# Kernel optimization log

Measured on AMD Instinct MI355X. Metric: run time of the kernel, lower is better.

## Reference

```python
import jax, jax.numpy as jnp
import numpy as np

# ---- module config (mirrors arch_args / init_kwargs) ----
W_BITS_PER_SLICE = 4      # slice_init=True -> weights quantized with STE to w_bits_per_slice
A_BITS = 8                # activation quantization bits
A_BITS_PER_STREAM = 8
VMAX = 1.0
GON_HW, GOFF_HW = 1.0, 1e-3   # weight_to_diff_conductance is called with Gon=1, Goff=1/1000 (hardcoded)
ADC_PREC = 8
ADC_STEP = 1e-3           # adc_static_step
NUM_SUBARRAYS = 9
SUB_SIZE = 256            # subarray_size; 256*3*3 / 256 = 9 even chunks
K, STRIDE, PAD = 3, 1, 1


def ste_quantize(x, bits):
    # Symmetric uniform quantizer with straight-through estimator (STE_Quantize).
    n = float(2 ** bits - 1)
    s = jnp.max(jnp.abs(x)) + 1e-12
    q = jnp.round(x / s * n) / n * s
    return x + jax.lax.stop_gradient(q - x)


def adc_quantize(I):
    # Nbit_ADC: static-step uniform ADC, signed (adc_pos_only=False), deterministic
    # rounding (adc_stoch_round=False), STE backward, no custom loss.
    half = 2 ** (ADC_PREC - 1)
    q = jnp.clip(jnp.round(I / ADC_STEP), -half, half - 1) * ADC_STEP
    return I + jax.lax.stop_gradient(q - I)


def setup_inputs():
    key = jax.random.key(0)
    k1, k2 = jax.random.split(key)
    x = jax.random.normal(k1, (32, 256, 32, 32), jnp.float32)
    fan_in = 256 * K * K
    w = jax.random.normal(k2, (256, 256, K, K), jnp.float32) * np.sqrt(2.0 / fan_in)  # kaiming_normal
    return {"inputs": x, "weight": w}


def reference(inputs, weight):
    B = inputs.shape[0]
    O = weight.shape[0]

    # forward(): quantize activations (a_bits) and weights (w_bits_per_slice, slice_init path)
    qa = ste_quantize(inputs, A_BITS)
    qw = ste_quantize(weight, W_BITS_PER_SLICE)

    # F.unfold -> [B, C*k*k, L], channel-major patch ordering (matches torch)
    patches = jax.lax.conv_general_dilated_patches(
        qa, (K, K), (STRIDE, STRIDE), ((PAD, PAD), (PAD, PAD)))
    Hp, Wp = patches.shape[2], patches.shape[3]
    L = Hp * Wp
    V = patches.reshape(B, NUM_SUBARRAYS, SUB_SIZE, L) * (VMAX / A_BITS_PER_STREAM)

    # Differential conductances: G_pos - G_neg. The dummy columns (both filled with
    # Goff) cancel exactly in I_pos - I_neg, so the net current per subarray is a
    # single contraction against qw * (Gon - Goff) / Nstates_slice.
    nstates = float(2 ** W_BITS_PER_SLICE - 1)
    Gd = qw.reshape(O, NUM_SUBARRAYS, SUB_SIZE) * ((GON_HW - GOFF_HW) / nstates)

    # per-subarray crossbar currents: [B, n_sub, O, L]
    I = jnp.einsum('bgfl,ogf->bgol', V, Gd)

    # shared ADC applied to each subarray output, then accumulate over subarrays
    accum = adc_quantize(I).sum(axis=1)  # [B, O, L]
    a_loss = jnp.float32(0.0)            # adc_custom_loss=False

    # F.fold with (1,1) kernel onto sqrt(L) x sqrt(L) grid == reshape
    result = accum.reshape(B, O, Hp, Wp)
    return (result, a_loss)
```

## Files before the change

kernel.cpp:

```cpp
#include <hip/hip_runtime.h>
#include <stdint.h>

typedef unsigned short u16;
typedef __attribute__((ext_vector_type(8))) short short8;
typedef __attribute__((ext_vector_type(4))) float floatx4;

#define NB 32
#define NC 256
#define NH 32
#define NW 32
#define NO 256
#define NPIX (NH*NW)
#define KPIX 9
#define NG 9
#define RUN 32
#define GK (NG*RUN)
#define KTOT (NG*GK)
#define PADH 34
#define PADSP (PADH*PADH)
#define QA_BSTRIDE (PADSP*NC)

#define AS1 __attribute__((address_space(1)))
#define AS3 __attribute__((address_space(3)))

__global__ void fused_pre(const float4* __restrict__ x4, int nx4,
                          const float4* __restrict__ w4, int nw4,
                          unsigned* __restrict__ outx, unsigned* __restrict__ outw,
                          u16* __restrict__ qa) {
  int bid = blockIdx.x;
  if (bid >= 1088) {
    int zb = bid - 1088;
    int b = zb / 9;
    int rem = (zb % 9) * 256 + threadIdx.x;
    if (rem >= 2112) return;
    int pb = rem >> 4, c16 = rem & 15;
    int y, x;
    if (pb < 68) { y = (pb >= 34) ? 33 : 0; x = pb % 34; }
    else { int q = pb - 68; y = 1 + (q >> 1); x = (q & 1) ? 33 : 0; }
    uint4 z; z.x = z.y = z.z = z.w = 0u;
    *(uint4*)(qa + ((size_t)(b * PADH + y) * PADH + x) * NC + c16 * 16) = z;
    return;
  }
  const float4* p; int n4; unsigned* out; int nb, b0;
  if (bid < 1024) { p = x4; n4 = nx4; out = outx; nb = 1024; b0 = bid; }
  else            { p = w4; n4 = nw4; out = outw; nb = 64;   b0 = bid - 1024; }
  float m = 0.f;
  for (int i = b0 * blockDim.x + threadIdx.x; i < n4; i += nb * blockDim.x) {
    float4 v = p[i];
    m = fmaxf(m, fmaxf(fmaxf(fabsf(v.x), fabsf(v.y)), fmaxf(fabsf(v.z), fabsf(v.w))));
  }
#pragma unroll
  for (int off = 32; off > 0; off >>= 1)
    m = fmaxf(m, __shfl_down(m, off, 64));
  __shared__ float sm[4];
  int lane = threadIdx.x & 63, wv = threadIdx.x >> 6;
  if (lane == 0) sm[wv] = m;
  __syncthreads();
  if (threadIdx.x == 0) {
    float mm = fmaxf(fmaxf(sm[0], sm[1]), fmaxf(sm[2], sm[3]));
    atomicMax(out, __float_as_uint(mm));
  }
}

__global__ void fused_quant(const float* __restrict__ x, const float* __restrict__ w,
                            const unsigned* __restrict__ scal,
                            u16* __restrict__ qa, u16* __restrict__ wq,
                            float* __restrict__ lossp) {
  int bid = blockIdx.x;
  if (bid < 8192) {
    __shared__ u16 t[32][33];
    double s = (double)__uint_as_float(scal[0]) + 1e-12;
    double inv = 255.0 / s;
    int tx = threadIdx.x & 31, ty = threadIdx.x >> 5;
    int ct = bid & 7, y = (bid >> 3) & 31, b = bid >> 8;
#pragma unroll
    for (int j = 0; j < 4; j++) {
      int cl = ty + j * 8;
      float v = x[(((size_t)b * NC + ct * 32 + cl) * NH + y) * NW + tx];
      double q = rint((double)v * inv);
      float qf = (float)q;
      t[cl][tx] = (u16)(__float_as_uint(qf) >> 16);
    }
    __syncthreads();
#pragma unroll
    for (int j = 0; j < 4; j++) {
      int xq = ty + j * 8;
      qa[((size_t)(b * PADH + y + 1) * PADH + (xq + 1)) * NC + ct * 32 + tx] = t[tx][xq];
    }
    return;
  }
  double s = (double)__uint_as_float(scal[1]) + 1e-12;
  double inv = 15.0 / s;
  int idx = (bid - 8192) * blockDim.x + threadIdx.x;
  if (idx == 0) *lossp = 0.0f;
  if (idx >= NO * KTOT) return;
  int o = idx / KTOT, kk = idx % KTOT;
  int g = kk / GK, rem = kk % GK;
  int r = rem / RUN, j = rem % RUN;
  int clo = (256 * g - r + 8) / 9;
  int chi = (256 * (g + 1) - r + 8) / 9; if (chi > NC) chi = NC;
  int cst = clo & ~3;
  int c = cst + j;
  float val = 0.f;
  if (c >= clo && c < chi) {
    float wv = w[((size_t)o * NC + c) * KPIX + r];
    val = (float)rint((double)wv * inv);
  }
  wq[idx] = (u16)(__float_as_uint(val) >> 16);
}

__global__ __launch_bounds__(128, 2) void gemm_adc(const u16* __restrict__ qa,
                                                   const u16* __restrict__ wq,
                                                   const unsigned* __restrict__ sc,
                                                   float* __restrict__ out) {
  __shared__ u16 lA[3 * 128 * RUN];
  __shared__ u16 lB[3 * 64 * RUN];
  const int tid = threadIdx.x;
  const int mblk = blockIdx.x, nblk = blockIdx.y;
  const int b = mblk >> 3;
  const int p0 = (mblk & 7) * 128;
  const int n0 = nblk * 64;
  const int lane = tid & 63, w = tid >> 6;
  const int fm = lane & 15, fq = lane >> 4;
  const int swz = (fq + ((fm >> 1) & 3)) & 3;

  double sa = (double)__uint_as_float(sc[0]) + 1e-12;
  double sw = (double)__uint_as_float(sc[1]) + 1e-12;
  double Sstep = sa * sw * 0.999 / 459.0;

  const int r0 = tid >> 2;
  const int jsrc = ((tid & 3) - ((tid >> 3) & 3)) & 3;
  const u16* Abase = qa + (size_t)b * QA_BSTRIDE
                     + (((p0 >> 5) + 1) * PADH + (r0 + 1)) * NC + jsrc * 8;
  const u16* Bbase = wq + (size_t)(n0 + r0) * KTOT + jsrc * 8;
  u16* Adst = &lA[tid * 8];
  u16* Bdst = &lB[tid * 8];

  floatx4 acc[4][4];
  float tot[4][4][4];
#pragma unroll
  for (int mi = 0; mi < 4; mi++)
#pragma unroll
    for (int ni = 0; ni < 4; ni++)
#pragma unroll
      for (int rr = 0; rr < 4; rr++) { acc[mi][ni][rr] = 0.f; tot[mi][ni][rr] = 0.f; }

#pragma unroll 1
  for (int g = 0; g < NG; g++) {
#pragma unroll 1
    for (int rc = 0; rc < 3; rc++) {
      int offA[3], kb[3];
#pragma unroll
      for (int ri = 0; ri < 3; ri++) {
        int r = rc * 3 + ri;
        int cst = ((256 * g - r + 8) / 9) & ~3;
        offA[ri] = ((rc - 1) * PADH + (ri - 1)) * NC + cst;
        kb[ri] = g * GK + r * RUN;
      }
#pragma unroll
      for (int ri = 0; ri < 3; ri++)
#pragma unroll
        for (int ii = 0; ii < 4; ii++)
          __builtin_amdgcn_global_load_lds(
              (const AS1 void*)(Abase + offA[ri] + ii * (PADH * NC)),
              (AS3 void*)(Adst + ri * 4096 + ii * 1024), 16, 0, 0);
#pragma unroll
      for (int ii = 0; ii < 6; ii++)
        __builtin_amdgcn_global_load_lds(
            (const AS1 void*)(Bbase + (ii & 1) * 32 * KTOT + kb[ii >> 1]),
            (AS3 void*)(Bdst + ii * 1024), 16, 0, 0);
      __syncthreads();
#pragma unroll
      for (int ri = 0; ri < 3; ri++) {
        short8 afr[4], bfr[4];
#pragma unroll
        for (int mi = 0; mi < 4; mi++)
          afr[mi] = *(const short8*)&lA[ri * 4096 + (w * 64 + mi * 16 + fm) * RUN + swz * 8];
#pragma unroll
        for (int ni = 0; ni < 4; ni++)
          bfr[ni] = *(const short8*)&lB[ri * 2048 + (ni * 16 + fm) * RUN + swz * 8];
#pragma unroll
        for (int mi = 0; mi < 4; mi++)
#pragma unroll
          for (int ni = 0; ni < 4; ni++)
            acc[mi][ni] = __builtin_amdgcn_mfma_f32_16x16x32_bf16(afr[mi], bfr[ni], acc[mi][ni], 0, 0, 0);
      }
      __syncthreads();
    }
#pragma unroll
    for (int mi = 0; mi < 4; mi++)
#pragma unroll
      for (int ni = 0; ni < 4; ni++)
#pragma unroll
        for (int rr = 0; rr < 4; rr++) {
          double d = (double)acc[mi][ni][rr] * Sstep;
          float tf = (float)rint(d);
          tf = fminf(fmaxf(tf, -128.f), 127.f);
          tot[mi][ni][rr] += tf;
          acc[mi][ni][rr] = 0.f;
        }
  }
#pragma unroll
  for (int mi = 0; mi < 4; mi++)
#pragma unroll
    for (int ni = 0; ni < 4; ni++) {
      int o = n0 + ni * 16 + fm;
      int p = p0 + w * 64 + mi * 16 + fq * 4;
      float4 o4;
      o4.x = tot[mi][ni][0] * 1e-3f;
      o4.y = tot[mi][ni][1] * 1e-3f;
      o4.z = tot[mi][ni][2] * 1e-3f;
      o4.w = tot[mi][ni][3] * 1e-3f;
      *(float4*)(out + ((size_t)(b * NO + o)) * NPIX + p) = o4;
    }
}

extern "C" void kernel_launch(void* const* d_in, const int* in_sizes, int n_in,
                              void* d_out, int out_size, void* d_ws, size_t ws_size,
                              hipStream_t stream) {
  const float* x = (const float*)d_in[0];
  const float* w = (const float*)d_in[1];
  float* out = (float*)d_out;

  unsigned* scal = (unsigned*)d_ws;
  u16* qa = (u16*)((char*)d_ws + 256);
  u16* wq = (u16*)((char*)d_ws + 256 + 18939904 + 8192);

  hipMemsetAsync(d_ws, 0, 256, stream);
  fused_pre<<<1376, 256, 0, stream>>>((const float4*)x, (NB * NC * NH * NW) / 4,
                                      (const float4*)w, (NO * NC * KPIX) / 4,
                                      scal, scal + 1, qa);
  fused_quant<<<8192 + 2592, 256, 0, stream>>>(x, w, scal, qa, wq, out + (out_size - 1));
  gemm_adc<<<dim3(256, 4), 128, 0, stream>>>(qa, wq, scal, out);
}
```

Before: 177.0 us.

## Double-buffer GEMM K-loop, replace atomic max with per-block partials, swap grid order

The GEMM main loop now walks 41 chunks of two kernel-pixel slices each and keeps two LDS buffers. The next chunk's async global-to-LDS loads are issued before the current chunk is computed, with explicit vmcnt waits, so memory traffic overlaps the MFMA work. The row stride of the weight matrix is padded to 2624 so the extra 82nd slice reads zeros. The global atomicMax and the memset are replaced by per-block partial maxima, which every block of the quant and GEMM kernels reduces again on its own. The grid is transposed so the N blocks sharing one A tile launch next to each other, which should improve L2 reuse. The costs are twice the LDS use, a redundant reduction in every block, and inline-asm waitcnt logic that is fragile.

Result: slower. 226.6 us (+28.1%).

```diff
diff --git a/kernel.cpp b/kernel.cpp
--- a/kernel.cpp
+++ b/kernel.cpp
@@ -16,6 +16,7 @@
 #define RUN 32
 #define GK (NG*RUN)
 #define KTOT (NG*GK)
+#define KSTORE 2624
 #define PADH 34
 #define PADSP (PADH*PADH)
 #define QA_BSTRIDE (PADSP*NC)
@@ -25,8 +26,7 @@
 
 __global__ void fused_pre(const float4* __restrict__ x4, int nx4,
                           const float4* __restrict__ w4, int nw4,
-                          unsigned* __restrict__ outx, unsigned* __restrict__ outw,
-                          u16* __restrict__ qa) {
+                          float* __restrict__ pmax, u16* __restrict__ qa) {
   int bid = blockIdx.x;
   if (bid >= 1088) {
     int zb = bid - 1088;
@@ -41,9 +41,9 @@
     *(uint4*)(qa + ((size_t)(b * PADH + y) * PADH + x) * NC + c16 * 16) = z;
     return;
   }
-  const float4* p; int n4; unsigned* out; int nb, b0;
-  if (bid < 1024) { p = x4; n4 = nx4; out = outx; nb = 1024; b0 = bid; }
-  else            { p = w4; n4 = nw4; out = outw; nb = 64;   b0 = bid - 1024; }
+  const float4* p; int n4; int nb, b0;
+  if (bid < 1024) { p = x4; n4 = nx4; nb = 1024; b0 = bid; }
+  else            { p = w4; n4 = nw4; nb = 64;   b0 = bid - 1024; }
   float m = 0.f;
   for (int i = b0 * blockDim.x + threadIdx.x; i < n4; i += nb * blockDim.x) {
     float4 v = p[i];
@@ -56,20 +56,46 @@
   int lane = threadIdx.x & 63, wv = threadIdx.x >> 6;
   if (lane == 0) sm[wv] = m;
   __syncthreads();
-  if (threadIdx.x == 0) {
-    float mm = fmaxf(fmaxf(sm[0], sm[1]), fmaxf(sm[2], sm[3]));
-    atomicMax(out, __float_as_uint(mm));
-  }
+  if (threadIdx.x == 0)
+    pmax[bid] = fmaxf(fmaxf(sm[0], sm[1]), fmaxf(sm[2], sm[3]));
+}
+
+__device__ inline void reduce_pmax(const float* pmax, int tid, int nthreads,
+                                   float* sred, float& mx_out, float& mw_out) {
+  const float4* pf4 = (const float4*)pmax;
+  float mx = 0.f, mw = 0.f;
+  for (int t = tid; t < 256; t += nthreads) {
+    float4 v = pf4[t];
+    mx = fmaxf(mx, fmaxf(fmaxf(v.x, v.y), fmaxf(v.z, v.w)));
+  }
+  if (tid < 16) {
+    float4 v = pf4[256 + tid];
+    mw = fmaxf(fmaxf(v.x, v.y), fmaxf(v.z, v.w));
+  }
+#pragma unroll
+  for (int off = 32; off > 0; off >>= 1) {
+    mx = fmaxf(mx, __shfl_down(mx, off, 64));
+    mw = fmaxf(mw, __shfl_down(mw, off, 64));
+  }
+  int lane = tid & 63, wv = tid >> 6, nw = nthreads >> 6;
+  if (lane == 0) { sred[wv] = mx; sred[8 + wv] = mw; }
+  __syncthreads();
+  mx = sred[0]; mw = sred[8];
+  for (int i = 1; i < nw; i++) { mx = fmaxf(mx, sred[i]); mw = fmaxf(mw, sred[8 + i]); }
+  mx_out = mx; mw_out = mw;
 }
 
 __global__ void fused_quant(const float* __restrict__ x, const float* __restrict__ w,
-                            const unsigned* __restrict__ scal,
+                            const float* __restrict__ pmax,
                             u16* __restrict__ qa, u16* __restrict__ wq,
                             float* __restrict__ lossp) {
+  __shared__ float sred[16];
+  float mx, mw;
+  reduce_pmax(pmax, threadIdx.x, 256, sred, mx, mw);
   int bid = blockIdx.x;
   if (bid < 8192) {
     __shared__ u16 t[32][33];
-    double s = (double)__uint_as_float(scal[0]) + 1e-12;
+    double s = (double)mx + 1e-12;
     double inv = 255.0 / s;
     int tx = threadIdx.x & 31, ty = threadIdx.x >> 5;
     int ct = bid & 7, y = (bid >> 3) & 31, b = bid >> 8;
@@ -89,52 +115,78 @@
     }
     return;
   }
-  double s = (double)__uint_as_float(scal[1]) + 1e-12;
+  double s = (double)mw + 1e-12;
   double inv = 15.0 / s;
   int idx = (bid - 8192) * blockDim.x + threadIdx.x;
   if (idx == 0) *lossp = 0.0f;
-  if (idx >= NO * KTOT) return;
-  int o = idx / KTOT, kk = idx % KTOT;
-  int g = kk / GK, rem = kk % GK;
-  int r = rem / RUN, j = rem % RUN;
-  int clo = (256 * g - r + 8) / 9;
-  int chi = (256 * (g + 1) - r + 8) / 9; if (chi > NC) chi = NC;
-  int cst = clo & ~3;
-  int c = cst + j;
+  if (idx >= NO * KSTORE) return;
+  int o = idx / KSTORE, kk = idx % KSTORE;
   float val = 0.f;
-  if (c >= clo && c < chi) {
-    float wv = w[((size_t)o * NC + c) * KPIX + r];
-    val = (float)rint((double)wv * inv);
+  if (kk < KTOT) {
+    int g = kk / GK, rem = kk % GK;
+    int r = rem / RUN, j = rem % RUN;
+    int clo = (256 * g - r + 8) / 9;
+    int chi = (256 * (g + 1) - r + 8) / 9; if (chi > NC) chi = NC;
+    int cst = clo & ~3;
+    int c = cst + j;
+    if (c >= clo && c < chi) {
+      float wv = w[((size_t)o * NC + c) * KPIX + r];
+      val = (float)rint((double)wv * inv);
+    }
   }
   wq[idx] = (u16)(__float_as_uint(val) >> 16);
 }
 
 __global__ __launch_bounds__(128, 2) void gemm_adc(const u16* __restrict__ qa,
                                                    const u16* __restrict__ wq,
-                                                   const unsigned* __restrict__ sc,
+                                                   const float* __restrict__ pmax,
                                                    float* __restrict__ out) {
-  __shared__ u16 lA[3 * 128 * RUN];
-  __shared__ u16 lB[3 * 64 * RUN];
+  __shared__ u16 lA[2 * 2 * 128 * RUN];
+  __shared__ u16 lB[2 * 2 * 64 * RUN];
+  __shared__ float sred[16];
   const int tid = threadIdx.x;
-  const int mblk = blockIdx.x, nblk = blockIdx.y;
+  float mx, mw;
+  reduce_pmax(pmax, tid, 128, sred, mx, mw);
+
+  const int nblk = blockIdx.x, mblk = blockIdx.y;
   const int b = mblk >> 3;
   const int p0 = (mblk & 7) * 128;
   const int n0 = nblk * 64;
-  const int lane = tid & 63, w = tid >> 6;
+  const int lane = tid & 63, wv = tid >> 6;
   const int fm = lane & 15, fq = lane >> 4;
   const int swz = (fq + ((fm >> 1) & 3)) & 3;
 
-  double sa = (double)__uint_as_float(sc[0]) + 1e-12;
-  double sw = (double)__uint_as_float(sc[1]) + 1e-12;
+  double sa = (double)mx + 1e-12;
+  double sw = (double)mw + 1e-12;
   double Sstep = sa * sw * 0.999 / 459.0;
 
   const int r0 = tid >> 2;
   const int jsrc = ((tid & 3) - ((tid >> 3) & 3)) & 3;
   const u16* Abase = qa + (size_t)b * QA_BSTRIDE
                      + (((p0 >> 5) + 1) * PADH + (r0 + 1)) * NC + jsrc * 8;
-  const u16* Bbase = wq + (size_t)(n0 + r0) * KTOT + jsrc * 8;
-  u16* Adst = &lA[tid * 8];
-  u16* Bdst = &lB[tid * 8];
+  const u16* Bbase = wq + (size_t)(n0 + r0) * KSTORE + jsrc * 8;
+
+  auto issue = [&](int c, int buf) {
+#pragma unroll
+    for (int rl = 0; rl < 2; rl++) {
+      int r = 2 * c + rl;
+      int ra = (r >= 81) ? 80 : r;
+      int g = ra / 9, rr = ra % 9;
+      int cst = ((256 * g - rr + 8) / 9) & ~3;
+      int offA = ((rr / 3 - 1) * PADH + (rr % 3 - 1)) * NC + cst;
+      int offB = r * RUN;
+      u16* Ad = &lA[buf * 8192 + rl * 4096 + tid * 8];
+      u16* Bd = &lB[buf * 4096 + rl * 2048 + tid * 8];
+#pragma unroll
+      for (int ii = 0; ii < 4; ii++)
+        __builtin_amdgcn_global_load_lds((const AS1 void*)(Abase + offA + ii * (PADH * NC)),
+                                         (AS3 void*)(Ad + ii * 1024), 16, 0, 0);
+#pragma unroll
+      for (int ii = 0; ii < 2; ii++)
+        __builtin_amdgcn_global_load_lds((const AS1 void*)(Bbase + offB + ii * 32 * KSTORE),
+                                         (AS3 void*)(Bd + ii * 1024), 16, 0, 0);
+    }
+  };
 
   floatx4 acc[4][4];
   float tot[4][4][4];
@@ -145,67 +197,60 @@
 #pragma unroll
       for (int rr = 0; rr < 4; rr++) { acc[mi][ni][rr] = 0.f; tot[mi][ni][rr] = 0.f; }
 
+  issue(0, 0);
 #pragma unroll 1
-  for (int g = 0; g < NG; g++) {
-#pragma unroll 1
-    for (int rc = 0; rc < 3; rc++) {
-      int offA[3], kb[3];
-#pragma unroll
-      for (int ri = 0; ri < 3; ri++) {
-        int r = rc * 3 + ri;
-        int cst = ((256 * g - r + 8) / 9) & ~3;
-        offA[ri] = ((rc - 1) * PADH + (ri - 1)) * NC + cst;
-        kb[ri] = g * GK + r * RUN;
+  for (int c = 0; c < 41; c++) {
+    if (c < 40) {
+      issue(c + 1, (c + 1) & 1);
+      asm volatile("s_waitcnt vmcnt(12)" ::: "memory");
+    } else {
+      asm volatile("s_waitcnt vmcnt(0)" ::: "memory");
+    }
+    __builtin_amdgcn_s_barrier();
+    asm volatile("" ::: "memory");
+    const int buf = c & 1;
+#pragma unroll
+    for (int rl = 0; rl < 2; rl++) {
+      const u16* pA = &lA[buf * 8192 + rl * 4096];
+      const u16* pB = &lB[buf * 4096 + rl * 2048];
+      short8 afr[4], bfr[4];
+#pragma unroll
+      for (int mi = 0; mi < 4; mi++)
+        afr[mi] = *(const short8*)&pA[(wv * 64 + mi * 16 + fm) * RUN + swz * 8];
+#pragma unroll
+      for (int ni = 0; ni < 4; ni++)
+        bfr[ni] = *(const short8*)&pB[(ni * 16 + fm) * RUN + swz * 8];
+#pragma unroll
+      for (int mi = 0; mi < 4; mi++)
+#pragma unroll
+        for (int ni = 0; ni < 4; ni++)
+          acc[mi][ni] = __builtin_amdgcn_mfma_f32_16x16x32_bf16(afr[mi], bfr[ni], acc[mi][ni], 0, 0, 0);
+      int r = 2 * c + rl;
+      if (r % 9 == 8) {
+#pragma unroll
+        for (int mi = 0; mi < 4; mi++)
+#pragma unroll
+          for (int ni = 0; ni < 4; ni++)
+#pragma unroll
+            for (int rr = 0; rr < 4; rr++) {
+              double d = (double)acc[mi][ni][rr] * Sstep;
+              float tf = (float)rint(d);
+              tf = fminf(fmaxf(tf, -128.f), 127.f);
+              tot[mi][ni][rr] += tf;
+              acc[mi][ni][rr] = 0.f;
+            }
       }
-#pragma unroll
-      for (int ri = 0; ri < 3; ri++)
-#pragma unroll
-        for (int ii = 0; ii < 4; ii++)
-          __builtin_amdgcn_global_load_lds(
-              (const AS1 void*)(Abase + offA[ri] + ii * (PADH * NC)),
-              (AS3 void*)(Adst + ri * 4096 + ii * 1024), 16, 0, 0);
-#pragma unroll
-      for (int ii = 0; ii < 6; ii++)
-        __builtin_amdgcn_global_load_lds(
-            (const AS1 void*)(Bbase + (ii & 1) * 32 * KTOT + kb[ii >> 1]),
-            (AS3 void*)(Bdst + ii * 1024), 16, 0, 0);
-      __syncthreads();
-#pragma unroll
-      for (int ri = 0; ri < 3; ri++) {
-        short8 afr[4], bfr[4];
-#pragma unroll
-        for (int mi = 0; mi < 4; mi++)
-          afr[mi] = *(const short8*)&lA[ri * 4096 + (w * 64 + mi * 16 + fm) * RUN + swz * 8];
-#pragma unroll
-        for (int ni = 0; ni < 4; ni++)
-          bfr[ni] = *(const short8*)&lB[ri * 2048 + (ni * 16 + fm) * RUN + swz * 8];
-#pragma unroll
-        for (int mi = 0; mi < 4; mi++)
-#pragma unroll
-          for (int ni = 0; ni < 4; ni++)
-            acc[mi][ni] = __builtin_amdgcn_mfma_f32_16x16x32_bf16(afr[mi], bfr[ni], acc[mi][ni], 0, 0, 0);
-      }
-      __syncthreads();
-    }
-#pragma unroll
-    for (int mi = 0; mi < 4; mi++)
-#pragma unroll
-      for (int ni = 0; ni < 4; ni++)
-#pragma unroll
-        for (int rr = 0; rr < 4; rr++) {
-          double d = (double)acc[mi][ni][rr] * Sstep;
-          float tf = (float)rint(d);
-          tf = fminf(fmaxf(tf, -128.f), 127.f);
-          tot[mi][ni][rr] += tf;
-          acc[mi][ni][rr] = 0.f;
-        }
+    }
+    asm volatile("" ::: "memory");
+    __builtin_amdgcn_s_barrier();
+    asm volatile("" ::: "memory");
   }
 #pragma unroll
   for (int mi = 0; mi < 4; mi++)
 #pragma unroll
     for (int ni = 0; ni < 4; ni++) {
       int o = n0 + ni * 16 + fm;
-      int p = p0 + w * 64 + mi * 16 + fq * 4;
+      int p = p0 + wv * 64 + mi * 16 + fq * 4;
       float4 o4;
       o4.x = tot[mi][ni][0] * 1e-3f;
       o4.y = tot[mi][ni][1] * 1e-3f;
@@ -222,14 +267,13 @@
   const float* w = (const float*)d_in[1];
   float* out = (float*)d_out;
 
-  unsigned* scal = (unsigned*)d_ws;
-  u16* qa = (u16*)((char*)d_ws + 256);
-  u16* wq = (u16*)((char*)d_ws + 256 + 18939904 + 8192);
-
-  hipMemsetAsync(d_ws, 0, 256, stream);
+  float* pmax = (float*)d_ws;
+  u16* qa = (u16*)((char*)d_ws + 8192);
+  u16* wq = (u16*)((char*)d_ws + 8192 + 18939904 + 8192);
+
   fused_pre<<<1376, 256, 0, stream>>>((const float4*)x, (NB * NC * NH * NW) / 4,
                                       (const float4*)w, (NO * NC * KPIX) / 4,
-                                      scal, scal + 1, qa);
-  fused_quant<<<8192 + 2592, 256, 0, stream>>>(x, w, scal, qa, wq, out + (out_size - 1));
-  gemm_adc<<<dim3(256, 4), 128, 0, stream>>>(qa, wq, scal, out);
-}
+                                      pmax, qa);
+  fused_quant<<<8192 + 2624, 256, 0, stream>>>(x, w, pmax, qa, wq, out + (out_size - 1));
+  gemm_adc<<<dim3(4, 256), 128, 0, stream>>>(qa, wq, pmax, out);
+}
```
